# Performance work log

Measured on AMD Instinct MI355X. Metric: run time of the kernel, lower is better.

## Reference

```python
import jax, jax.numpy as jnp
import numpy as np

B, H, W, C = 2, 128, 128, 128
NS = 8                      # attn_num_splits
WH, WW = H // NS, W // NS   # window size 16x16
SH, SW = WH // 2, WW // 2   # shift sizes
HID = 2 * C * 4             # ffn hidden (in_channels = 2*d_model, expansion 4)
EPS = 1e-5


def _make_swin_mask():
    # Standard shifted-window attention mask: -100 between different regions.
    img = np.zeros((H, W), np.int32)
    cnt = 0
    for hs in (slice(0, -WH), slice(-WH, -SH), slice(-SH, None)):
        for ws in (slice(0, -WW), slice(-WW, -SW), slice(-SW, None)):
            img[hs, ws] = cnt
            cnt += 1
    ids = img.reshape(NS, WH, NS, WW).transpose(0, 2, 1, 3).reshape(NS * NS, WH * WW)
    mask = np.where(ids[:, None, :] != ids[:, :, None], -100.0, 0.0).astype(np.float32)
    return jnp.asarray(mask)  # (64, 256, 256)


def _layernorm(x, g, b):
    m = jnp.mean(x, axis=-1, keepdims=True)
    v = jnp.mean(jnp.square(x - m), axis=-1, keepdims=True)
    return (x - m) * jax.lax.rsqrt(v + EPS) * g + b


def setup_inputs() -> dict:
    key = jax.random.key(0)
    ks = jax.random.split(key, 8)
    s = 1.0 / np.sqrt(C)
    return {
        "source": jax.random.normal(ks[0], (B, H * W, C), jnp.float32),
        "target": jax.random.normal(ks[1], (B, H * W, C), jnp.float32),
        "Wq": jax.random.normal(ks[2], (C, C), jnp.float32) * s,
        "Wk": jax.random.normal(ks[3], (C, C), jnp.float32) * s,
        "Wv": jax.random.normal(ks[4], (C, C), jnp.float32) * s,
        "Wm": jax.random.normal(ks[5], (C, C), jnp.float32) * s,
        "g1": jnp.ones((C,), jnp.float32),
        "b1": jnp.zeros((C,), jnp.float32),
        "W1": jax.random.normal(ks[6], (2 * C, HID), jnp.float32) * (1.0 / np.sqrt(2 * C)),
        "W2": jax.random.normal(ks[7], (HID, C), jnp.float32) * (1.0 / np.sqrt(HID)),
        "g2": jnp.ones((C,), jnp.float32),
        "b2": jnp.zeros((C,), jnp.float32),
        "shifted_window_attn_mask": _make_swin_mask(),
        "height": H,
        "width": W,
        "attn_num_splits": NS,
    }


def reference(source, target, Wq, Wk, Wv, Wm, g1, b1, W1, W2, g2, b2,
              shifted_window_attn_mask, height, width, attn_num_splits):
    b, L, c = source.shape
    h, w, ns = height, width, attn_num_splits
    wh, ww = h // ns, w // ns
    sh, sw = wh // 2, ww // 2

    q = source @ Wq
    k = target @ Wk
    v = target @ Wv

    def to_windows(x):
        # (b, h*w, c) -> shifted -> (b, nWin, wh*ww, c)
        x = x.reshape(b, h, w, c)
        x = jnp.roll(x, (-sh, -sw), axis=(1, 2))
        x = x.reshape(b, ns, wh, ns, ww, c).transpose(0, 1, 3, 2, 4, 5)
        return x.reshape(b, ns * ns, wh * ww, c)

    qw, kw, vw = to_windows(q), to_windows(k), to_windows(v)
    scores = jnp.einsum('bnlc,bnmc->bnlm', qw, kw) / (c ** 0.5)
    scores = scores + shifted_window_attn_mask[None]  # broadcast over batch
    attn = jax.nn.softmax(scores, axis=-1)
    out = jnp.einsum('bnlm,bnmc->bnlc', attn, vw)

    # merge windows back and undo the shift
    out = out.reshape(b, ns, ns, wh, ww, c).transpose(0, 1, 3, 2, 4, 5).reshape(b, h, w, c)
    out = jnp.roll(out, (sh, sw), axis=(1, 2)).reshape(b, h * w, c)

    message = _layernorm(out @ Wm, g1, b1)
    ffn_in = jnp.concatenate([source, message], axis=-1)
    message = jax.nn.gelu(ffn_in @ W1, approximate=False) @ W2
    message = _layernorm(message, g2, b2)
    return source + message
```

## Files before the change

kernel.cpp:

```cpp
#include <hip/hip_runtime.h>
#include <math.h>
#include <stdint.h>


typedef unsigned short u16;
typedef __attribute__((ext_vector_type(8))) short bf16x8;
typedef __attribute__((ext_vector_type(4))) float f32x4;
typedef __attribute__((ext_vector_type(4))) short u16x4;

__device__ __forceinline__ u16 f2b(float f) {
    unsigned int i = __float_as_uint(f);
    unsigned int r = (i + 0x7fffu + ((i >> 16) & 1u)) >> 16;
    return (u16)r;
}

__device__ __forceinline__ float gelu_e(float x) {
    float y = fabsf(x) * 0.70710678118f;
    float u = fmaf(y, fmaf(y, fmaf(y, fmaf(y, 0.078108f, 0.000972f),
                                   0.230389f), 0.278393f), 1.0f);
    u = u * u; u = u * u;
    float r = __builtin_amdgcn_rcpf(u);
    return fmaxf(x, 0.f) - 0.5f * fabsf(x) * r;
}

__device__ __forceinline__ void cp16(const void* g, void* l) {
    auto* gp = reinterpret_cast<const __attribute__((address_space(1))) unsigned int*>(
        reinterpret_cast<uintptr_t>(g));
    auto* lp = reinterpret_cast<__attribute__((address_space(3))) unsigned int*>(
        reinterpret_cast<uintptr_t>(l));
    __builtin_amdgcn_global_load_lds(gp, lp, 16, 0, 0);
}

__device__ __forceinline__ int win_map(int gm) {
    int b = gm >> 14, rr = gm & 16383;
    int win = rr >> 8, t = rr & 255;
    int wi = win >> 3, wj = win & 7, i = t >> 4, j = t & 15;
    int h = (wi * 16 + i + 8) & 127;
    int w = (wj * 16 + j + 8) & 127;
    return (b << 14) + h * 128 + w;
}

__global__ __launch_bounds__(256, 2)
void gemm_qkv(const u16* __restrict__ srcb, const u16* __restrict__ tgtb,
              const u16* __restrict__ Bt, u16* __restrict__ qw,
              u16* __restrict__ kw, u16* __restrict__ vwt)
{
    __shared__ __align__(16) u16 SMEM[32768];
    u16* As = SMEM;
    u16* Bs = SMEM + 16384;
    u16* Ts = SMEM;

    const int tid = threadIdx.x;
    const int w = tid >> 6, lane = tid & 63;
    const int lm = lane & 15, q = lane >> 4;
    const int wm = w >> 1, wn = w & 1;
    const int m0 = blockIdx.x * 128;
    const int y = blockIdx.y;
    const u16* Ab = (y == 0) ? srcb : tgtb;

#pragma unroll
    for (int s = 0; s < 4; ++s)
#pragma unroll
        for (int i = 0; i < 2; ++i) {
            int row = w * 32 + i * 16 + (lane >> 2);
            int kc = s * 32 + (lane & 3) * 8;
            cp16(Ab + (size_t)win_map(m0 + row) * 128 + kc,
                 (void*)(As + (s * 128 + w * 32 + i * 16) * 32));
            cp16(Bt + (size_t)(y * 128 + row) * 128 + kc,
                 (void*)(Bs + (s * 128 + w * 32 + i * 16) * 32));
        }
    __syncthreads();

    f32x4 acc[4][4] = {};
#pragma unroll
    for (int s = 0; s < 4; ++s) {
        bf16x8 af[4], bfr[4];
#pragma unroll
        for (int t = 0; t < 4; ++t)
            af[t] = *(const bf16x8*)(As + (s * 128 + wm * 64 + t * 16 + lm) * 32 + q * 8);
#pragma unroll
        for (int t = 0; t < 4; ++t)
            bfr[t] = *(const bf16x8*)(Bs + (s * 128 + wn * 64 + t * 16 + lm) * 32 + q * 8);
#pragma unroll
        for (int mt = 0; mt < 4; ++mt)
#pragma unroll
            for (int nt = 0; nt < 4; ++nt)
                acc[mt][nt] = __builtin_amdgcn_mfma_f32_16x16x32_bf16(
                    af[mt], bfr[nt], acc[mt][nt], 0, 0, 0);
    }

    __syncthreads();
#pragma unroll
    for (int mt = 0; mt < 4; ++mt)
#pragma unroll
        for (int nt = 0; nt < 4; ++nt)
#pragma unroll
            for (int r = 0; r < 4; ++r) {
                int rowl = wm * 64 + mt * 16 + q * 4 + r;
                int col = wn * 64 + nt * 16 + lm;
                int idx = (y == 2) ? col * 136 + rowl : rowl * 136 + col;
                Ts[idx] = f2b(acc[mt][nt][r]);
            }
    __syncthreads();
    const int c8 = (tid & 15) * 8;
#pragma unroll
    for (int i = 0; i < 8; ++i) {
        int rr = i * 16 + (tid >> 4);
        bf16x8 t = *(const bf16x8*)(Ts + rr * 136 + c8);
        if (y == 2) {
            int wix = m0 >> 8, tok0 = m0 & 255;
            *(bf16x8*)(vwt + (size_t)wix * 32768 + (size_t)rr * 256 + tok0 + c8) = t;
        } else {
            u16* Cv = (y == 0) ? qw : kw;
            *(bf16x8*)(Cv + (size_t)(m0 + rr) * 128 + c8) = t;
        }
    }
}

__global__ __launch_bounds__(256, 2)
void attn_msg(const u16* __restrict__ qw, const u16* __restrict__ kw,
              const u16* __restrict__ vt, const u16* __restrict__ wmt,
              const float* __restrict__ g, const float* __restrict__ bb,
              u16* __restrict__ msgb)
{
    __shared__ __align__(16) u16 Ps[64 * 264];
    __shared__ __align__(16) u16 B32[16384];

    const int tid = threadIdx.x, w = tid >> 6, lane = tid & 63;
    const int lm = lane & 15, q = lane >> 4;
    const int l4r = lane >> 2, l4c = (lane & 3) * 8;
    const int bid = blockIdx.x;
    const int qc = bid & 3, win = (bid >> 2) & 63, b = bid >> 8;
    const int wi = win >> 3, wj = win & 7;
    const int q0 = qc * 64;
    const size_t wbase = (size_t)(b * 64 + win);
    const u16* kwb = kw + wbase * 256 * 128;
    const u16* qwb = qw + wbase * 256 * 128;
    const u16* vtb = vt + wbase * 128 * 256;

    u16* Qs = Ps;
#pragma unroll
    for (int i = 0; i < 4; ++i)
        cp16(qwb + (size_t)(q0 + w * 16 + l4r) * 128 + i * 32 + l4c,
             (void*)(Qs + (i * 64 + w * 16) * 32));
#pragma unroll
    for (int s = 0; s < 4; ++s)
#pragma unroll
        for (int i = 0; i < 2; ++i) {
            int tok = w * 32 + i * 16 + l4r;
            cp16(kwb + (size_t)tok * 128 + s * 32 + l4c,
                 (void*)(B32 + (s * 128 + w * 32 + i * 16) * 32));
        }
    __syncthreads();

    bf16x8 af[4];
#pragma unroll
    for (int kt = 0; kt < 4; ++kt)
        af[kt] = *(const bf16x8*)(Qs + (kt * 64 + w * 16 + lm) * 32 + q * 8);

    f32x4 s[16];
#pragma unroll
    for (int nt = 0; nt < 16; ++nt) { f32x4 z = {0.f, 0.f, 0.f, 0.f}; s[nt] = z; }
#pragma unroll
    for (int kt = 0; kt < 4; ++kt)
#pragma unroll
        for (int nt = 0; nt < 8; ++nt) {
            bf16x8 bf = *(const bf16x8*)(B32 + (kt * 128 + nt * 16 + lm) * 32 + q * 8);
            s[nt] = __builtin_amdgcn_mfma_f32_16x16x32_bf16(af[kt], bf, s[nt], 0, 0, 0);
        }
    __syncthreads();
#pragma unroll
    for (int ss = 0; ss < 4; ++ss)
#pragma unroll
        for (int i = 0; i < 2; ++i) {
            int tok = 128 + w * 32 + i * 16 + l4r;
            cp16(kwb + (size_t)tok * 128 + ss * 32 + l4c,
                 (void*)(B32 + (ss * 128 + w * 32 + i * 16) * 32));
        }
    __syncthreads();
#pragma unroll
    for (int kt = 0; kt < 4; ++kt)
#pragma unroll
        for (int nt = 8; nt < 16; ++nt) {
            bf16x8 bf = *(const bf16x8*)(B32 + (kt * 128 + (nt - 8) * 16 + lm) * 32 + q * 8);
            s[nt] = __builtin_amdgcn_mfma_f32_16x16x32_bf16(af[kt], bf, s[nt], 0, 0, 0);
        }
    __syncthreads();

#pragma unroll
    for (int tt = 0; tt < 4; ++tt)
#pragma unroll
        for (int i = 0; i < 2; ++i) {
            int ch = w * 32 + i * 16 + l4r;
            cp16(vtb + (size_t)ch * 256 + tt * 32 + l4c,
                 (void*)(B32 + (tt * 128 + w * 32 + i * 16) * 32));
        }

    int idk[16];
#pragma unroll
    for (int nt = 0; nt < 16; ++nt) {
        int rh = (wi == 7) ? ((nt >= 8) ? 2 : 1) : 0;
        int rw = (wj == 7) ? ((lm >= 8) ? 2 : 1) : 0;
        idk[nt] = rh * 3 + rw;
    }
    const float scale = 0.08838834764831845f;
#pragma unroll
    for (int r = 0; r < 4; ++r) {
        int tq = q0 + w * 16 + q * 4 + r;
        int iq = tq >> 4, jq = tq & 15;
        int rhq = (wi == 7) ? ((iq >= 8) ? 2 : 1) : 0;
        int rwq = (wj == 7) ? ((jq >= 8) ? 2 : 1) : 0;
        int idq = rhq * 3 + rwq;
        float sv[16];
        float mx = -1e30f;
#pragma unroll
        for (int nt = 0; nt < 16; ++nt) {
            float x = s[nt][r] * scale + ((idq != idk[nt]) ? -100.f : 0.f);
            sv[nt] = x; mx = fmaxf(mx, x);
        }
        mx = fmaxf(mx, __shfl_xor(mx, 1));
        mx = fmaxf(mx, __shfl_xor(mx, 2));
        mx = fmaxf(mx, __shfl_xor(mx, 4));
        mx = fmaxf(mx, __shfl_xor(mx, 8));
        float sum = 0.f;
#pragma unroll
        for (int nt = 0; nt < 16; ++nt) { float e = __expf(sv[nt] - mx); sv[nt] = e; sum += e; }
        sum += __shfl_xor(sum, 1);
        sum += __shfl_xor(sum, 2);
        sum += __shfl_xor(sum, 4);
        sum += __shfl_xor(sum, 8);
        float inv = 1.0f / sum;
#pragma unroll
        for (int nt = 0; nt < 16; ++nt)
            Ps[(w * 16 + q * 4 + r) * 264 + nt * 16 + lm] = f2b(sv[nt] * inv);
    }
    __syncthreads();

    f32x4 o[8];
#pragma unroll
    for (int nt = 0; nt < 8; ++nt) { f32x4 z = {0.f, 0.f, 0.f, 0.f}; o[nt] = z; }
#pragma unroll
    for (int tt = 0; tt < 4; ++tt) {
        bf16x8 pf = *(const bf16x8*)(Ps + (w * 16 + lm) * 264 + tt * 32 + q * 8);
#pragma unroll
        for (int nt = 0; nt < 8; ++nt) {
            bf16x8 vf = *(const bf16x8*)(B32 + (tt * 128 + nt * 16 + lm) * 32 + q * 8);
            o[nt] = __builtin_amdgcn_mfma_f32_16x16x32_bf16(pf, vf, o[nt], 0, 0, 0);
        }
    }
    __syncthreads();
#pragma unroll
    for (int tt = 0; tt < 4; ++tt)
#pragma unroll
        for (int i = 0; i < 2; ++i) {
            int ch = w * 32 + i * 16 + l4r;
            cp16(vtb + (size_t)ch * 256 + 128 + tt * 32 + l4c,
                 (void*)(B32 + (tt * 128 + w * 32 + i * 16) * 32));
        }
    __syncthreads();
#pragma unroll
    for (int tt = 4; tt < 8; ++tt) {
        bf16x8 pf = *(const bf16x8*)(Ps + (w * 16 + lm) * 264 + tt * 32 + q * 8);
#pragma unroll
        for (int nt = 0; nt < 8; ++nt) {
            bf16x8 vf = *(const bf16x8*)(B32 + ((tt - 4) * 128 + nt * 16 + lm) * 32 + q * 8);
            o[nt] = __builtin_amdgcn_mfma_f32_16x16x32_bf16(pf, vf, o[nt], 0, 0, 0);
        }
    }
    __syncthreads();

#pragma unroll
    for (int ss = 0; ss < 4; ++ss)
#pragma unroll
        for (int i = 0; i < 2; ++i) {
            int n = w * 32 + i * 16 + l4r;
            cp16(wmt + (size_t)n * 128 + ss * 32 + l4c,
                 (void*)(B32 + (ss * 128 + w * 32 + i * 16) * 32));
        }
    u16* Ot = Ps;
#pragma unroll
    for (int r = 0; r < 4; ++r) {
        int rl = w * 16 + q * 4 + r;
#pragma unroll
        for (int nt = 0; nt < 8; ++nt)
            Ot[rl * 136 + nt * 16 + lm] = f2b(o[nt][r]);
    }
    __syncthreads();

    f32x4 macc[8];
#pragma unroll
    for (int n2 = 0; n2 < 8; ++n2) { f32x4 z = {0.f, 0.f, 0.f, 0.f}; macc[n2] = z; }
#pragma unroll
    for (int kt = 0; kt < 4; ++kt) {
        bf16x8 paf = *(const bf16x8*)(Ot + (w * 16 + lm) * 136 + kt * 32 + q * 8);
#pragma unroll
        for (int n2 = 0; n2 < 8; ++n2) {
            bf16x8 wf = *(const bf16x8*)(B32 + (kt * 128 + n2 * 16 + lm) * 32 + q * 8);
            macc[n2] = __builtin_amdgcn_mfma_f32_16x16x32_bf16(paf, wf, macc[n2], 0, 0, 0);
        }
    }

    float gv[8], bv[8];
#pragma unroll
    for (int n2 = 0; n2 < 8; ++n2) {
        int col = n2 * 16 + lm;
        gv[n2] = g[col]; bv[n2] = bb[col];
    }
#pragma unroll
    for (int r = 0; r < 4; ++r) {
        float s1 = 0.f, s2 = 0.f;
#pragma unroll
        for (int n2 = 0; n2 < 8; ++n2) {
            float v = macc[n2][r];
            s1 += v; s2 += v * v;
        }
        s1 += __shfl_xor(s1, 1); s2 += __shfl_xor(s2, 1);
        s1 += __shfl_xor(s1, 2); s2 += __shfl_xor(s2, 2);
        s1 += __shfl_xor(s1, 4); s2 += __shfl_xor(s2, 4);
        s1 += __shfl_xor(s1, 8); s2 += __shfl_xor(s2, 8);
        float mean = s1 * (1.f / 128.f);
        float var = fmaxf(s2 * (1.f / 128.f) - mean * mean, 0.f);
        float rs = rsqrtf(var + 1e-5f);
        int t = q0 + w * 16 + q * 4 + r;
        int ii = t >> 4, jj = t & 15;
        int h = (wi * 16 + ii + 8) & 127;
        int w2 = (wj * 16 + jj + 8) & 127;
        size_t orow = ((size_t)b * 16384 + h * 128 + w2) * 128;
#pragma unroll
        for (int n2 = 0; n2 < 8; ++n2)
            msgb[orow + n2 * 16 + lm] = f2b((macc[n2][r] - mean) * rs * gv[n2] + bv[n2]);
    }
}

__global__ __launch_bounds__(512, 2)
void fused_ffn(const u16* __restrict__ A0, const u16* __restrict__ A1,
               const u16* __restrict__ W1T, const u16* __restrict__ W2T,
               const float* __restrict__ g, const float* __restrict__ bb,
               const float* __restrict__ resid, float* __restrict__ outv)
{
    __shared__ __align__(16) u16 As[32768];
    __shared__ __align__(16) u16 W1s[16384];
    __shared__ __align__(16) u16 W2s[16384];
    __shared__ __align__(16) u16 Gs[8192];

    const int tid = threadIdx.x;
    const int w = tid >> 6, lane = tid & 63;
    const int lm = lane & 15, q = lane >> 4;
    const int l4r = lane >> 2, l4c = (lane & 3) * 8;
    const int wm = w >> 1, wn = w & 1;
    const int m0 = blockIdx.x * 128;

    {
        const u16* Ab = (w < 4) ? A0 : A1;
        int kc = (w & 3) * 32 + l4c;
#pragma unroll
        for (int i = 0; i < 8; ++i)
            cp16(Ab + (size_t)(m0 + i * 16 + l4r) * 128 + kc,
                 (void*)(As + (w * 128 + i * 16) * 32));
    }
#pragma unroll
    for (int i = 0; i < 4; ++i)
        cp16(W1T + (size_t)(i * 16 + l4r) * 256 + w * 32 + l4c,
             (void*)(W1s + (w * 64 + i * 16) * 32));
    {
        int s2 = w >> 2, rg = w & 3;
#pragma unroll
        for (int i = 0; i < 2; ++i)
            cp16(W2T + (size_t)(rg * 32 + i * 16 + l4r) * 1024 + s2 * 32 + l4c,
                 (void*)(W2s + (s2 * 128 + rg * 32 + i * 16) * 32));
    }
    __syncthreads();

    f32x4 acc2[2][4] = {};
    for (int c = 0; c < 16; ++c) {
        f32x4 acc1[2][2] = {};
#pragma unroll
        for (int s = 0; s < 8; ++s) {
            bf16x8 af[2], bf[2];
#pragma unroll
            for (int mt = 0; mt < 2; ++mt)
                af[mt] = *(const bf16x8*)(As + (s * 128 + wm * 32 + mt * 16 + lm) * 32 + q * 8);
#pragma unroll
            for (int nt = 0; nt < 2; ++nt)
                bf[nt] = *(const bf16x8*)(W1s + (s * 64 + wn * 32 + nt * 16 + lm) * 32 + q * 8);
#pragma unroll
            for (int mt = 0; mt < 2; ++mt)
#pragma unroll
                for (int nt = 0; nt < 2; ++nt)
                    acc1[mt][nt] = __builtin_amdgcn_mfma_f32_16x16x32_bf16(
                        af[mt], bf[nt], acc1[mt][nt], 0, 0, 0);
        }

#pragma unroll
        for (int mt = 0; mt < 2; ++mt)
#pragma unroll
            for (int nt = 0; nt < 2; ++nt)
#pragma unroll
                for (int r = 0; r < 4; ++r) {
                    int row = wm * 32 + mt * 16 + q * 4 + r;
                    int col = wn * 32 + nt * 16 + lm;
                    int idx = row * 64 + ((((col >> 3) ^ (row & 7))) << 3) + (col & 7);
                    Gs[idx] = f2b(gelu_e(acc1[mt][nt][r]));
                }
        __syncthreads();

        if (c + 1 < 16) {
#pragma unroll
            for (int i = 0; i < 4; ++i)
                cp16(W1T + (size_t)((c + 1) * 64 + i * 16 + l4r) * 256 + w * 32 + l4c,
                     (void*)(W1s + (w * 64 + i * 16) * 32));
            int s2 = w >> 2, rg = w & 3;
            int st = (c + 1) & 1;
#pragma unroll
            for (int i = 0; i < 2; ++i)
                cp16(W2T + (size_t)(rg * 32 + i * 16 + l4r) * 1024
                         + (c + 1) * 64 + s2 * 32 + l4c,
                     (void*)(W2s + st * 8192 + (s2 * 128 + rg * 32 + i * 16) * 32));
        }

        const u16* W2p = W2s + (c & 1) * 8192;
#pragma unroll
        for (int ks = 0; ks < 2; ++ks) {
            bf16x8 pa[2], wf[4];
#pragma unroll
            for (int mt = 0; mt < 2; ++mt) {
                int row = wm * 32 + mt * 16 + lm;
                pa[mt] = *(const bf16x8*)(Gs + row * 64
                                          + ((((ks << 2) + q) ^ (row & 7)) << 3));
            }
#pragma unroll
            for (int nt = 0; nt < 4; ++nt)
                wf[nt] = *(const bf16x8*)(W2p + (ks * 128 + wn * 64 + nt * 16 + lm) * 32 + q * 8);
#pragma unroll
            for (int mt = 0; mt < 2; ++mt)
#pragma unroll
                for (int nt = 0; nt < 4; ++nt)
                    acc2[mt][nt] = __builtin_amdgcn_mfma_f32_16x16x32_bf16(
                        pa[mt], wf[nt], acc2[mt][nt], 0, 0, 0);
        }
        __syncthreads();
    }

    float* stats = (float*)Gs;
#pragma unroll
    for (int mt = 0; mt < 2; ++mt)
#pragma unroll
        for (int r = 0; r < 4; ++r) {
            float s1 = 0.f, s2 = 0.f;
#pragma unroll
            for (int nt = 0; nt < 4; ++nt) {
                float v = acc2[mt][nt][r];
                s1 += v; s2 += v * v;
            }
            s1 += __shfl_xor(s1, 1); s2 += __shfl_xor(s2, 1);
            s1 += __shfl_xor(s1, 2); s2 += __shfl_xor(s2, 2);
            s1 += __shfl_xor(s1, 4); s2 += __shfl_xor(s2, 4);
            s1 += __shfl_xor(s1, 8); s2 += __shfl_xor(s2, 8);
            if (lm == 0) {
                int row = wm * 32 + mt * 16 + q * 4 + r;
                stats[row * 4 + wn * 2] = s1;
                stats[row * 4 + wn * 2 + 1] = s2;
            }
        }
    __syncthreads();

    float gv[4], bv[4];
#pragma unroll
    for (int nt = 0; nt < 4; ++nt) {
        int col = wn * 64 + nt * 16 + lm;
        gv[nt] = g[col]; bv[nt] = bb[col];
    }
#pragma unroll
    for (int mt = 0; mt < 2; ++mt)
#pragma unroll
        for (int r = 0; r < 4; ++r) {
            int row = wm * 32 + mt * 16 + q * 4 + r;
            f32x4 st = *(const f32x4*)(stats + row * 4);
            float mean = (st[0] + st[2]) * (1.f / 128.f);
            float var = fmaxf((st[1] + st[3]) * (1.f / 128.f) - mean * mean, 0.f);
            float rs = rsqrtf(var + 1e-5f);
#pragma unroll
            for (int nt = 0; nt < 4; ++nt) {
                int col = wn * 64 + nt * 16 + lm;
                size_t gi = (size_t)(m0 + row) * 128 + col;
                outv[gi] = (acc2[mt][nt][r] - mean) * rs * gv[nt] + bv[nt] + resid[gi];
            }
        }
}

__global__ void prep_all(const float* __restrict__ Wq, const float* __restrict__ Wk,
                         const float* __restrict__ Wv, const float* __restrict__ Wm,
                         const float* __restrict__ W1, const float* __restrict__ W2,
                         const float* __restrict__ src, const float* __restrict__ tgt,
                         u16* __restrict__ ws, u16* __restrict__ srcb,
                         u16* __restrict__ tgtb)
{
    int bx = blockIdx.x;
    if (bx < 1792) {
        int idx = bx * 256 + threadIdx.x;
        if (idx < 65536) {
            int m = idx >> 14, e = idx & 16383;
            const float* sp = (m == 0) ? Wq : (m == 1) ? Wk : (m == 2) ? Wv : Wm;
            int n = e >> 7, k = e & 127;
            ws[m * 16384 + n * 128 + k] = f2b(sp[k * 128 + n]);
        } else if (idx < 327680) {
            int e = idx - 65536;
            int n = e >> 8, k = e & 255;
            ws[65536 + n * 256 + k] = f2b(W1[k * 1024 + n]);
        } else {
            int e = idx - 327680;
            int n = e >> 10, k = e & 1023;
            ws[327680 + n * 1024 + k] = f2b(W2[k * 128 + n]);
        }
    } else {
        int idx = (bx - 1792) * 256 + threadIdx.x;
        const float* s; u16* d; int i;
        if (idx < 1048576) { s = src; d = srcb; i = idx * 4; }
        else               { s = tgt; d = tgtb; i = (idx - 1048576) * 4; }
        f32x4 v = *(const f32x4*)(s + i);
        u16x4 o; o[0] = f2b(v[0]); o[1] = f2b(v[1]); o[2] = f2b(v[2]); o[3] = f2b(v[3]);
        *(u16x4*)(d + i) = o;
    }
}

#define OFF_WQT  0u
#define OFF_WMT  49152u
#define OFF_W1T  65536u
#define OFF_W2T  327680u
#define OFF_SRCB 458752u
#define OFF_TGTB 4653056u
#define OFF_QW   8847360u
#define OFF_KW   13041664u
#define OFF_VWT  17235968u
#define OFF_MSGB 21430272u

extern "C" void kernel_launch(void* const* d_in, const int* in_sizes, int n_in,
                              void* d_out, int out_size, void* d_ws, size_t ws_size,
                              hipStream_t stream)
{
    (void)in_sizes; (void)n_in; (void)out_size; (void)ws_size;
    const float* source = (const float*)d_in[0];
    const float* target = (const float*)d_in[1];
    const float* Wq = (const float*)d_in[2];
    const float* Wk = (const float*)d_in[3];
    const float* Wv = (const float*)d_in[4];
    const float* Wm = (const float*)d_in[5];
    const float* g1 = (const float*)d_in[6];
    const float* b1 = (const float*)d_in[7];
    const float* W1 = (const float*)d_in[8];
    const float* W2 = (const float*)d_in[9];
    const float* g2 = (const float*)d_in[10];
    const float* b2 = (const float*)d_in[11];
    u16* ws = (u16*)d_ws;
    float* out = (float*)d_out;

    prep_all<<<9984, 256, 0, stream>>>(Wq, Wk, Wv, Wm, W1, W2, source, target,
                                       ws, ws + OFF_SRCB, ws + OFF_TGTB);
    gemm_qkv<<<dim3(256, 3), 256, 0, stream>>>(
        ws + OFF_SRCB, ws + OFF_TGTB, ws + OFF_WQT,
        ws + OFF_QW, ws + OFF_KW, ws + OFF_VWT);
    attn_msg<<<512, 256, 0, stream>>>(
        ws + OFF_QW, ws + OFF_KW, ws + OFF_VWT, ws + OFF_WMT, g1, b1,
        ws + OFF_MSGB);
    fused_ffn<<<256, 512, 0, stream>>>(
        ws + OFF_SRCB, ws + OFF_MSGB, ws + OFF_W1T, ws + OFF_W2T,
        g2, b2, source, out);
}
```

Measured before the change: 199.8 us.

## Restructure fused FFN: 16 waves, A operands in registers, double-buffered W1

The fused FFN kernel now runs 1024 threads (16 waves) per block instead of 512. Each wave keeps its A-tile fragments in registers, loaded straight from global memory, so the shared-memory As buffer goes away. That frees LDS to double-buffer W1, and the next chunk's W1/W2 are prefetched at the start of each iteration. The first GEMM swaps its operands so each lane holds consecutive hidden columns, and GELU outputs are packed with v_cvt_pk_bf16_f32 into 64-bit LDS stores. The goal is more waves to hide latency and fewer LDS reads and stores, at the cost of higher register pressure and only one block per CU.

```diff
diff --git a/kernel.cpp b/kernel.cpp
--- a/kernel.cpp
+++ b/kernel.cpp
@@ -7,6 +7,7 @@
 typedef __attribute__((ext_vector_type(8))) short bf16x8;
 typedef __attribute__((ext_vector_type(4))) float f32x4;
 typedef __attribute__((ext_vector_type(4))) short u16x4;
+typedef __attribute__((ext_vector_type(2))) unsigned int u32x2;
 
 __device__ __forceinline__ u16 f2b(float f) {
     unsigned int i = __float_as_uint(f);
@@ -332,14 +333,13 @@
     }
 }
 
-__global__ __launch_bounds__(512, 2)
+__global__ __launch_bounds__(1024, 4)
 void fused_ffn(const u16* __restrict__ A0, const u16* __restrict__ A1,
                const u16* __restrict__ W1T, const u16* __restrict__ W2T,
                const float* __restrict__ g, const float* __restrict__ bb,
                const float* __restrict__ resid, float* __restrict__ outv)
 {
-    __shared__ __align__(16) u16 As[32768];
-    __shared__ __align__(16) u16 W1s[16384];
+    __shared__ __align__(16) u16 W1s[32768];
     __shared__ __align__(16) u16 W2s[16384];
     __shared__ __align__(16) u16 Gs[8192];
 
@@ -347,94 +347,81 @@
     const int w = tid >> 6, lane = tid & 63;
     const int lm = lane & 15, q = lane >> 4;
     const int l4r = lane >> 2, l4c = (lane & 3) * 8;
-    const int wm = w >> 1, wn = w & 1;
+    const int wm = w >> 2, wn = w & 3;
     const int m0 = blockIdx.x * 128;
 
-    {
-        const u16* Ab = (w < 4) ? A0 : A1;
-        int kc = (w & 3) * 32 + l4c;
-#pragma unroll
-        for (int i = 0; i < 8; ++i)
-            cp16(Ab + (size_t)(m0 + i * 16 + l4r) * 128 + kc,
-                 (void*)(As + (w * 128 + i * 16) * 32));
-    }
-#pragma unroll
-    for (int i = 0; i < 4; ++i)
-        cp16(W1T + (size_t)(i * 16 + l4r) * 256 + w * 32 + l4c,
-             (void*)(W1s + (w * 64 + i * 16) * 32));
-    {
-        int s2 = w >> 2, rg = w & 3;
-#pragma unroll
-        for (int i = 0; i < 2; ++i)
-            cp16(W2T + (size_t)(rg * 32 + i * 16 + l4r) * 1024 + s2 * 32 + l4c,
-                 (void*)(W2s + (s2 * 128 + rg * 32 + i * 16) * 32));
-    }
-    __syncthreads();
-
-    f32x4 acc2[2][4] = {};
+    const int s_ks = w >> 1, s_hh = (w & 1) * 32;
+    const int s_s2 = w >> 3, s_rg = w & 7;
+
+    bf16x8 areg[2][8];
+#pragma unroll
+    for (int mt = 0; mt < 2; ++mt)
+#pragma unroll
+        for (int ks = 0; ks < 8; ++ks) {
+            const u16* Ab = (ks < 4) ? A0 : A1;
+            areg[mt][ks] = *(const bf16x8*)(
+                Ab + (size_t)(m0 + wm * 32 + mt * 16 + lm) * 128 + (ks & 3) * 32 + q * 8);
+        }
+#pragma unroll
+    for (int i = 0; i < 2; ++i)
+        cp16(W1T + (size_t)(s_hh + i * 16 + l4r) * 256 + s_ks * 32 + l4c,
+             (void*)(W1s + (s_ks * 64 + s_hh + i * 16) * 32));
+    cp16(W2T + (size_t)(s_rg * 16 + l4r) * 1024 + s_s2 * 32 + l4c,
+         (void*)(W2s + (s_s2 * 128 + s_rg * 16) * 32));
+    __syncthreads();
+
+    f32x4 acc2[2][2] = {};
     for (int c = 0; c < 16; ++c) {
-        f32x4 acc1[2][2] = {};
-#pragma unroll
-        for (int s = 0; s < 8; ++s) {
-            bf16x8 af[2], bf[2];
+        const int cur = c & 1;
+        const u16* W1c = W1s + cur * 16384;
+        const u16* W2c = W2s + cur * 8192;
+        if (c < 15) {
+            u16* W1n = W1s + (cur ^ 1) * 16384;
+            u16* W2n = W2s + (cur ^ 1) * 8192;
+#pragma unroll
+            for (int i = 0; i < 2; ++i)
+                cp16(W1T + (size_t)((c + 1) * 64 + s_hh + i * 16 + l4r) * 256 + s_ks * 32 + l4c,
+                     (void*)(W1n + (s_ks * 64 + s_hh + i * 16) * 32));
+            cp16(W2T + (size_t)(s_rg * 16 + l4r) * 1024 + (c + 1) * 64 + s_s2 * 32 + l4c,
+                 (void*)(W2n + (s_s2 * 128 + s_rg * 16) * 32));
+        }
+        f32x4 acc1[2] = {};
+#pragma unroll
+        for (int ks = 0; ks < 8; ++ks) {
+            bf16x8 w1f = *(const bf16x8*)(W1c + (ks * 64 + wn * 16 + lm) * 32 + q * 8);
 #pragma unroll
             for (int mt = 0; mt < 2; ++mt)
-                af[mt] = *(const bf16x8*)(As + (s * 128 + wm * 32 + mt * 16 + lm) * 32 + q * 8);
+                acc1[mt] = __builtin_amdgcn_mfma_f32_16x16x32_bf16(
+                    w1f, areg[mt][ks], acc1[mt], 0, 0, 0);
+        }
+#pragma unroll
+        for (int mt = 0; mt < 2; ++mt) {
+            float g0 = gelu_e(acc1[mt][0]), g1 = gelu_e(acc1[mt][1]);
+            float g2 = gelu_e(acc1[mt][2]), g3 = gelu_e(acc1[mt][3]);
+            unsigned p0, p1;
+            asm("v_cvt_pk_bf16_f32 %0, %1, %2" : "=v"(p0) : "v"(g0), "v"(g1));
+            asm("v_cvt_pk_bf16_f32 %0, %1, %2" : "=v"(p1) : "v"(g2), "v"(g3));
+            int tok = wm * 32 + mt * 16 + lm;
+            int slot = (wn * 2 + (q >> 1)) ^ (tok & 7);
+            u32x2 pk; pk[0] = p0; pk[1] = p1;
+            *(u32x2*)(Gs + tok * 64 + slot * 8 + (q & 1) * 4) = pk;
+        }
+        __syncthreads();
+#pragma unroll
+        for (int ks = 0; ks < 2; ++ks) {
+            bf16x8 pa[2], wf[2];
+#pragma unroll
+            for (int mt = 0; mt < 2; ++mt) {
+                int tok = wm * 32 + mt * 16 + lm;
+                pa[mt] = *(const bf16x8*)(Gs + tok * 64 + (((ks * 4 + q) ^ (tok & 7)) * 8));
+            }
 #pragma unroll
             for (int nt = 0; nt < 2; ++nt)
-                bf[nt] = *(const bf16x8*)(W1s + (s * 64 + wn * 32 + nt * 16 + lm) * 32 + q * 8);
+                wf[nt] = *(const bf16x8*)(W2c + (ks * 128 + wn * 32 + nt * 16 + lm) * 32 + q * 8);
 #pragma unroll
             for (int mt = 0; mt < 2; ++mt)
 #pragma unroll
                 for (int nt = 0; nt < 2; ++nt)
-                    acc1[mt][nt] = __builtin_amdgcn_mfma_f32_16x16x32_bf16(
-                        af[mt], bf[nt], acc1[mt][nt], 0, 0, 0);
-        }
-
-#pragma unroll
-        for (int mt = 0; mt < 2; ++mt)
-#pragma unroll
-            for (int nt = 0; nt < 2; ++nt)
-#pragma unroll
-                for (int r = 0; r < 4; ++r) {
-                    int row = wm * 32 + mt * 16 + q * 4 + r;
-                    int col = wn * 32 + nt * 16 + lm;
-                    int idx = row * 64 + ((((col >> 3) ^ (row & 7))) << 3) + (col & 7);
-                    Gs[idx] = f2b(gelu_e(acc1[mt][nt][r]));
-                }
-        __syncthreads();
-
-        if (c + 1 < 16) {
-#pragma unroll
-            for (int i = 0; i < 4; ++i)
-                cp16(W1T + (size_t)((c + 1) * 64 + i * 16 + l4r) * 256 + w * 32 + l4c,
-                     (void*)(W1s + (w * 64 + i * 16) * 32));
-            int s2 = w >> 2, rg = w & 3;
-            int st = (c + 1) & 1;
-#pragma unroll
-            for (int i = 0; i < 2; ++i)
-                cp16(W2T + (size_t)(rg * 32 + i * 16 + l4r) * 1024
-                         + (c + 1) * 64 + s2 * 32 + l4c,
-                     (void*)(W2s + st * 8192 + (s2 * 128 + rg * 32 + i * 16) * 32));
-        }
-
-        const u16* W2p = W2s + (c & 1) * 8192;
-#pragma unroll
-        for (int ks = 0; ks < 2; ++ks) {
-            bf16x8 pa[2], wf[4];
-#pragma unroll
-            for (int mt = 0; mt < 2; ++mt) {
-                int row = wm * 32 + mt * 16 + lm;
-                pa[mt] = *(const bf16x8*)(Gs + row * 64
-                                          + ((((ks << 2) + q) ^ (row & 7)) << 3));
-            }
-#pragma unroll
-            for (int nt = 0; nt < 4; ++nt)
-                wf[nt] = *(const bf16x8*)(W2p + (ks * 128 + wn * 64 + nt * 16 + lm) * 32 + q * 8);
-#pragma unroll
-            for (int mt = 0; mt < 2; ++mt)
-#pragma unroll
-                for (int nt = 0; nt < 4; ++nt)
                     acc2[mt][nt] = __builtin_amdgcn_mfma_f32_16x16x32_bf16(
                         pa[mt], wf[nt], acc2[mt][nt], 0, 0, 0);
         }
@@ -448,7 +435,7 @@
         for (int r = 0; r < 4; ++r) {
             float s1 = 0.f, s2 = 0.f;
 #pragma unroll
-            for (int nt = 0; nt < 4; ++nt) {
+            for (int nt = 0; nt < 2; ++nt) {
                 float v = acc2[mt][nt][r];
                 s1 += v; s2 += v * v;
             }
@@ -458,16 +445,16 @@
             s1 += __shfl_xor(s1, 8); s2 += __shfl_xor(s2, 8);
             if (lm == 0) {
                 int row = wm * 32 + mt * 16 + q * 4 + r;
-                stats[row * 4 + wn * 2] = s1;
-                stats[row * 4 + wn * 2 + 1] = s2;
+                stats[row * 8 + wn * 2] = s1;
+                stats[row * 8 + wn * 2 + 1] = s2;
             }
         }
     __syncthreads();
 
-    float gv[4], bv[4];
-#pragma unroll
-    for (int nt = 0; nt < 4; ++nt) {
-        int col = wn * 64 + nt * 16 + lm;
+    float gv[2], bv[2];
+#pragma unroll
+    for (int nt = 0; nt < 2; ++nt) {
+        int col = wn * 32 + nt * 16 + lm;
         gv[nt] = g[col]; bv[nt] = bb[col];
     }
 #pragma unroll
@@ -475,13 +462,16 @@
 #pragma unroll
         for (int r = 0; r < 4; ++r) {
             int row = wm * 32 + mt * 16 + q * 4 + r;
-            f32x4 st = *(const f32x4*)(stats + row * 4);
-            float mean = (st[0] + st[2]) * (1.f / 128.f);
-            float var = fmaxf((st[1] + st[3]) * (1.f / 128.f) - mean * mean, 0.f);
+            f32x4 st0 = *(const f32x4*)(stats + row * 8);
+            f32x4 st1 = *(const f32x4*)(stats + row * 8 + 4);
+            float s1 = st0[0] + st0[2] + st1[0] + st1[2];
+            float s2 = st0[1] + st0[3] + st1[1] + st1[3];
+            float mean = s1 * (1.f / 128.f);
+            float var = fmaxf(s2 * (1.f / 128.f) - mean * mean, 0.f);
             float rs = rsqrtf(var + 1e-5f);
 #pragma unroll
-            for (int nt = 0; nt < 4; ++nt) {
-                int col = wn * 64 + nt * 16 + lm;
+            for (int nt = 0; nt < 2; ++nt) {
+                int col = wn * 32 + nt * 16 + lm;
                 size_t gi = (size_t)(m0 + row) * 128 + col;
                 outv[gi] = (acc2[mt][nt][r] - mean) * rs * gv[nt] + bv[nt] + resid[gi];
             }
@@ -562,7 +552,7 @@
     attn_msg<<<512, 256, 0, stream>>>(
         ws + OFF_QW, ws + OFF_KW, ws + OFF_VWT, ws + OFF_WMT, g1, b1,
         ws + OFF_MSGB);
-    fused_ffn<<<256, 512, 0, stream>>>(
+    fused_ffn<<<256, 1024, 0, stream>>>(
         ws + OFF_SRCB, ws + OFF_MSGB, ws + OFF_W1T, ws + OFF_W2T,
         g2, b2, source, out);
 }
```

After: 192.2 us. 3.8% less time.
